# Optimization experiments

Hardware: AMD Instinct MI355X
Metric: run time of the kernel (lower is better)

Reference implementation:

```python
import jax, jax.numpy as jnp
import numpy as np

EPS = 1e-7  # K.epsilon()

def squash(s):
    # s: [B, J, D]
    sq_norm = jnp.sum(jnp.square(s), axis=-1, keepdims=True)
    scale = sq_norm / (1.0 + sq_norm) / jnp.sqrt(sq_norm + EPS)
    return scale * s

def setup_inputs() -> dict:
    key = jax.random.key(0)
    k1, k2 = jax.random.split(key)
    B, I, Din = 128, 2048, 8
    J, D = 16, 16
    inputs = jax.random.normal(k1, (B, I, Din), dtype=jnp.float32)
    # glorot-uniform-ish scale for W
    limit = np.sqrt(6.0 / (Din + D)).astype(np.float32)
    W = jax.random.uniform(k2, (J, I, D, Din), dtype=jnp.float32, minval=-limit, maxval=limit)
    return {"inputs": inputs, "W": W}

def reference(inputs, W):
    # inputs: [B, I, Din]; W: [J, I, D, Din]
    num_routings = 3
    # inputs_hat[b,j,i,d] = sum_f W[j,i,d,f] * inputs[b,i,f]
    u_hat = jnp.einsum('bif,jidf->bjid', inputs, W)  # [B, J, I, D]
    B, J, I, D = u_hat.shape
    b = jnp.zeros((B, J, I), dtype=u_hat.dtype)
    v = None
    for r in range(num_routings):
        c = jax.nn.softmax(b, axis=1)                 # softmax over output capsules (dim=1)
        s = jnp.einsum('bji,bjid->bjd', c, u_hat)     # weighted sum over input capsules
        v = squash(s)                                 # [B, J, D]
        if r < num_routings - 1:
            b = b + jnp.einsum('bjd,bjid->bji', v, u_hat)  # agreement update
    return v
```

## Files before the change

### kernel.cpp

```cpp
#include <hip/hip_runtime.h>
#include <math.h>

#define B_   128
#define I_   2048
#define F_   8
#define J_   16
#define D_   16
#define JD   256
#define IT   16
#define NIT  (I_/IT)
#define BT   16
#define NBG  (B_/BT)
#define SROW 257

typedef _Float16 f16;
typedef _Float16 f16x8 __attribute__((ext_vector_type(8)));
typedef float    f32x4 __attribute__((ext_vector_type(4)));

#if defined(__has_builtin)
#  if __has_builtin(__builtin_amdgcn_permlane32_swap)
#    define HAVE_PLS32 1
#  endif
#endif

template <int CTRL>
__device__ __forceinline__ float dpp_add(float v) {
    int t = __builtin_amdgcn_update_dpp(0, __float_as_int(v), CTRL, 0xF, 0xF, true);
    return v + __int_as_float(t);
}
__device__ __forceinline__ float row_sum16(float v) {
    v = dpp_add<0x128>(v);
    v = dpp_add<0x124>(v);
    v = dpp_add<0x122>(v);
    v = dpp_add<0x121>(v);
    return v;
}

__device__ __forceinline__ float fold16(float p) {
    return p + __int_as_float(__builtin_amdgcn_ds_swizzle(__float_as_int(p), 0x401F));
}
__device__ __forceinline__ float fold32(float p) {
#ifdef HAVE_PLS32
    auto r = __builtin_amdgcn_permlane32_swap(__float_as_int(p), __float_as_int(p),
                                              false, false);
    return __int_as_float(r[0]) + __int_as_float(r[1]);
#else
    return p + __shfl_xor(p, 32);
#endif
}

__device__ __forceinline__ f16x8 cvt8(float4 a0, float4 a1) {
    f16x8 h = {(f16)a0.x, (f16)a0.y, (f16)a0.z, (f16)a0.w,
               (f16)a1.x, (f16)a1.y, (f16)a1.z, (f16)a1.w};
    return h;
}

__global__ __launch_bounds__(256) void caps_pass0(
    const float* __restrict__ Wf,
    const float* __restrict__ xf,
    f16* __restrict__ Wt,
    f16* __restrict__ xt,
    f16* __restrict__ sp)
{
    const int it = blockIdx.x, bg = blockIdx.y;
    const int i0 = it * IT, b0 = bg * BT;
    const int t = threadIdx.x;
    const int w = t >> 6, l = t & 63;
    const int lb = l & 15, lq = l >> 4;

    __shared__ f16   xlds[IT][BT][F_];
    __shared__ float slds[BT * SROW];

    {
        const int b = t >> 4, i = t & 15;
        const size_t off = ((size_t)(b0 + b) * I_ + i0 + i) * F_;
        const float4* src = reinterpret_cast<const float4*>(xf + off);
        f16x8 h = cvt8(src[0], src[1]);
        *reinterpret_cast<f16x8*>(xt + off) = h;
        *reinterpret_cast<f16x8*>(&xlds[i][b][0]) = h;
    }
    __syncthreads();

    const f32x4 zero = {0.f, 0.f, 0.f, 0.f};
    f32x4 sacc[4] = {zero, zero, zero, zero};

    #pragma unroll
    for (int m = 0; m < 4; ++m) {
        const int i = m * 4 + lq;
        f16x8 xv = *reinterpret_cast<const f16x8*>(&xlds[i][lb][0]);
        #pragma unroll
        for (int jj = 0; jj < 4; ++jj) {
            const size_t off =
                (((size_t)(w * 4 + jj) * I_ + i0 + i) * D_ + lb) * F_;
            const float4* sw = reinterpret_cast<const float4*>(Wf + off);
            f16x8 af = cvt8(sw[0], sw[1]);
            if (bg == 0) *reinterpret_cast<f16x8*>(Wt + off) = af;
            sacc[jj] = __builtin_amdgcn_mfma_f32_16x16x32_f16(
                af, xv, sacc[jj], 0, 0, 0);
        }
    }

    #pragma unroll
    for (int jj = 0; jj < 4; ++jj) {
        f32x4 sv = sacc[jj] * 0.0625f;
        const int j = w * 4 + jj;
        #pragma unroll
        for (int r = 0; r < 4; ++r)
            slds[lb * SROW + j * D_ + lq * 4 + r] = sv[r];
    }
    __syncthreads();
    {
        const int b = t >> 4, seg = t & 15;
        float o[16];
        #pragma unroll
        for (int k = 0; k < 16; ++k)
            o[k] = slds[b * SROW + seg * 16 + k];
        f16x8 o0 = {(f16)o[0], (f16)o[1], (f16)o[2],  (f16)o[3],
                    (f16)o[4], (f16)o[5], (f16)o[6],  (f16)o[7]};
        f16x8 o1 = {(f16)o[8], (f16)o[9], (f16)o[10], (f16)o[11],
                    (f16)o[12], (f16)o[13], (f16)o[14], (f16)o[15]};
        f16* dst = sp + ((size_t)it * B_ + b0 + b) * JD + seg * 16;
        *reinterpret_cast<f16x8*>(dst) = o0;
        *reinterpret_cast<f16x8*>(dst + 8) = o1;
    }
}

__global__ __launch_bounds__(256) void caps_pass1(
    const f16* __restrict__ Wt,
    const f16* __restrict__ xt,
    const float* __restrict__ vsum,
    f16* __restrict__ sp)
{
    const int it = blockIdx.x, bg = blockIdx.y;
    const int i0 = it * IT, b0 = bg * BT;
    const int t = threadIdx.x;
    const int w = t >> 6, l = t & 63;
    const int lb = l & 15, lq = l >> 4;

    __shared__ f16 xlds[IT][BT][F_];
    __shared__ union {
        float cl[J_ * IT * BT];
        float slds[BT * SROW];
    } sh;

    {
        const int b = t >> 4, i = t & 15;
        f16x8 v = *reinterpret_cast<const f16x8*>(
            xt + ((size_t)(b0 + b) * I_ + i0 + i) * F_);
        *reinterpret_cast<f16x8*>(&xlds[i][b][0]) = v;
    }

    const f16* wp[4];
    #pragma unroll
    for (int jj = 0; jj < 4; ++jj)
        wp[jj] = Wt + (((size_t)(w * 4 + jj) * I_ + i0) * D_ + lb) * F_;

    const f32x4 zero = {0.f, 0.f, 0.f, 0.f};
    f32x4 sacc[4] = {zero, zero, zero, zero};

    float4 vr[4];
    #pragma unroll
    for (int jj = 0; jj < 4; ++jj)
        vr[jj] = *reinterpret_cast<const float4*>(
            vsum + (size_t)(b0 + lb) * JD + (w * 4 + jj) * D_ + lq * 4);
    __syncthreads();

    #pragma unroll 4
    for (int il = 0; il < IT; ++il) {
        f16x8 bf = {0, 0, 0, 0, 0, 0, 0, 0};
        if (l < 16) bf = *reinterpret_cast<const f16x8*>(&xlds[il][lb][0]);
        #pragma unroll
        for (int jj = 0; jj < 4; ++jj) {
            f16x8 af = *reinterpret_cast<const f16x8*>(wp[jj] + il * (D_ * F_));
            f32x4 u = __builtin_amdgcn_mfma_f32_16x16x32_f16(af, bf, zero, 0, 0, 0);
            float p = u[0] * vr[jj].x + u[1] * vr[jj].y +
                      u[2] * vr[jj].z + u[3] * vr[jj].w;
            p = fold32(fold16(p));
            if (l < 16) sh.cl[(((w * 4 + jj) * IT) + il) * BT + lb] = p;
        }
    }
    __syncthreads();

    {
        const int i = t >> 4, b = t & 15;
        float e[J_];
        float mx = -1e30f;
        #pragma unroll
        for (int j = 0; j < J_; ++j) {
            e[j] = sh.cl[(j * IT + i) * BT + b];
            mx = fmaxf(mx, e[j]);
        }
        float ssum = 0.f;
        #pragma unroll
        for (int j = 0; j < J_; ++j) { e[j] = __expf(e[j] - mx); ssum += e[j]; }
        const float inv = 1.f / ssum;
        #pragma unroll
        for (int j = 0; j < J_; ++j) sh.cl[(j * IT + i) * BT + b] = e[j] * inv;
    }
    __syncthreads();

    #pragma unroll
    for (int m = 0; m < 4; ++m) {
        const int i = m * 4 + lq;
        f16x8 xv = *reinterpret_cast<const f16x8*>(&xlds[i][lb][0]);
        #pragma unroll
        for (int jj = 0; jj < 4; ++jj) {
            const f16 ch = (f16)sh.cl[(((w * 4 + jj) * IT) + i) * BT + lb];
            f16x8 bf = xv * ch;
            f16x8 af = *reinterpret_cast<const f16x8*>(wp[jj] + i * (D_ * F_));
            sacc[jj] = __builtin_amdgcn_mfma_f32_16x16x32_f16(
                af, bf, sacc[jj], 0, 0, 0);
        }
    }
    __syncthreads();

    #pragma unroll
    for (int jj = 0; jj < 4; ++jj) {
        const int j = w * 4 + jj;
        #pragma unroll
        for (int r = 0; r < 4; ++r)
            sh.slds[lb * SROW + j * D_ + lq * 4 + r] = sacc[jj][r];
    }
    __syncthreads();
    {
        const int b = t >> 4, seg = t & 15;
        float o[16];
        #pragma unroll
        for (int k = 0; k < 16; ++k)
            o[k] = sh.slds[b * SROW + seg * 16 + k];
        f16x8 o0 = {(f16)o[0], (f16)o[1], (f16)o[2],  (f16)o[3],
                    (f16)o[4], (f16)o[5], (f16)o[6],  (f16)o[7]};
        f16x8 o1 = {(f16)o[8], (f16)o[9], (f16)o[10], (f16)o[11],
                    (f16)o[12], (f16)o[13], (f16)o[14], (f16)o[15]};
        f16* dst = sp + ((size_t)it * B_ + b0 + b) * JD + seg * 16;
        *reinterpret_cast<f16x8*>(dst) = o0;
        *reinterpret_cast<f16x8*>(dst + 8) = o1;
    }
}

template <int MODE>
__global__ __launch_bounds__(512) void caps_reduce(
    const f16* __restrict__ sp,
    const float* __restrict__ vA,
    float* __restrict__ vout)
{
    const int b = blockIdx.x, jh = blockIdx.y;
    const int t = threadIdx.x;
    const int g = t >> 4, c8 = t & 15;
    constexpr int ITS = NIT / 32;

    float acc[8] = {0.f, 0.f, 0.f, 0.f, 0.f, 0.f, 0.f, 0.f};
    const f16* base = sp + ((size_t)(g * ITS) * B_ + b) * JD + jh * 128 + c8 * 8;
    #pragma unroll
    for (int k = 0; k < ITS; ++k) {
        f16x8 v = *reinterpret_cast<const f16x8*>(base + (size_t)k * B_ * JD);
        #pragma unroll
        for (int e = 0; e < 8; ++e) acc[e] += (float)v[e];
    }

    __shared__ float lds[32][128];
    #pragma unroll
    for (int e = 0; e < 8; ++e) lds[g][c8 * 8 + e] = acc[e];
    __syncthreads();

    if (t < 128) {
        float a = 0.f;
        #pragma unroll
        for (int gg = 0; gg < 32; ++gg) a += lds[gg][t];
        const float sq = row_sum16(a * a);
        const float scale = sq / (1.f + sq) * rsqrtf(sq + 1e-7f);
        float v = scale * a;
        const int jd = jh * 128 + t;
        if (MODE == 1) v += vA[(size_t)b * JD + jd];
        vout[(size_t)b * JD + jd] = v;
    }
}

extern "C" void kernel_launch(void* const* d_in, const int* in_sizes, int n_in,
                              void* d_out, int out_size, void* d_ws,
                              size_t ws_size, hipStream_t stream) {
    const float* x = (const float*)d_in[0];
    const float* W = (const float*)d_in[1];
    float* out = (float*)d_out;

    const size_t NW = (size_t)J_ * I_ * D_ * F_;
    const size_t NX = (size_t)B_ * I_ * F_;
    const size_t NSP = (size_t)NIT * B_ * JD;

    f16* Wt = (f16*)d_ws;
    f16* xt = Wt + NW;
    f16* sp = xt + NX;
    float* vA = (float*)(sp + NSP);
    float* vB = vA + (size_t)B_ * JD;

    dim3 grid(NIT, NBG), blk(256);
    dim3 rgrid(B_, 2), rblk(512);

    caps_pass0<<<grid, blk, 0, stream>>>(W, x, Wt, xt, sp);
    caps_reduce<0><<<rgrid, rblk, 0, stream>>>(sp, nullptr, vA);
    caps_pass1<<<grid, blk, 0, stream>>>(Wt, xt, vA, sp);
    caps_reduce<1><<<rgrid, rblk, 0, stream>>>(sp, vA, vB);
    caps_pass1<<<grid, blk, 0, stream>>>(Wt, xt, vB, sp);
    caps_reduce<2><<<rgrid, rblk, 0, stream>>>(sp, nullptr, out);
}
```

Before: 82.33 us.

## Fuse cross-block reduction into pass kernels via last-arriver atomic ticket

Drops the three separate caps_reduce launches. Each pass kernel now takes an atomic ticket at its end, and the last 64 blocks to arrive spin until all blocks finish, then perform the reduction and squash for two batch rows each. This removes launch gaps and the tail of the separate reduce kernels, at the cost of a memset launch, spin-waiting blocks, and a reduction carried out by only 64 blocks.

```diff
diff --git a/kernel.cpp b/kernel.cpp
--- a/kernel.cpp
+++ b/kernel.cpp
@@ -11,6 +11,9 @@
 #define NIT  (I_/IT)
 #define BT   16
 #define NBG  (B_/BT)
+#define GRID_TOT (NIT*NBG)
+#define NRED 64
+#define RB   2
 #define SROW 257
 
 typedef _Float16 f16;
@@ -22,19 +25,6 @@
 #    define HAVE_PLS32 1
 #  endif
 #endif
-
-template <int CTRL>
-__device__ __forceinline__ float dpp_add(float v) {
-    int t = __builtin_amdgcn_update_dpp(0, __float_as_int(v), CTRL, 0xF, 0xF, true);
-    return v + __int_as_float(t);
-}
-__device__ __forceinline__ float row_sum16(float v) {
-    v = dpp_add<0x128>(v);
-    v = dpp_add<0x124>(v);
-    v = dpp_add<0x122>(v);
-    v = dpp_add<0x121>(v);
-    return v;
-}
 
 __device__ __forceinline__ float fold16(float p) {
     return p + __int_as_float(__builtin_amdgcn_ds_swizzle(__float_as_int(p), 0x401F));
@@ -55,12 +45,82 @@
     return h;
 }
 
+template <int MODE>
+__device__ __forceinline__ void tail_reduce(
+    const f16* __restrict__ sp,
+    const float* __restrict__ vAin,
+    float* __restrict__ vout,
+    int* __restrict__ cnt,
+    float* __restrict__ scratch,
+    int* __restrict__ tick_s,
+    const int t)
+{
+    __syncthreads();
+    if (t == 0)
+        *tick_s = __hip_atomic_fetch_add(cnt, 1, __ATOMIC_ACQ_REL,
+                                         __HIP_MEMORY_SCOPE_AGENT);
+    __syncthreads();
+    const int ticket = *tick_s;
+    if (ticket < GRID_TOT - NRED) return;
+
+    if (t == 0) {
+        while (__hip_atomic_load(cnt, __ATOMIC_ACQUIRE,
+                                 __HIP_MEMORY_SCOPE_AGENT) < GRID_TOT)
+            __builtin_amdgcn_s_sleep(8);
+    }
+    __syncthreads();
+
+    const int rblk = ticket - (GRID_TOT - NRED);
+    const int q = t >> 6, c = t & 63;
+    const int bb = c >> 5, jd8 = c & 31;
+    const int b = rblk * RB + bb;
+
+    float acc[8] = {0.f, 0.f, 0.f, 0.f, 0.f, 0.f, 0.f, 0.f};
+    const f16* base = sp + ((size_t)(q * 32) * B_ + b) * JD + jd8 * 8;
+    #pragma unroll 8
+    for (int k = 0; k < 32; ++k) {
+        f16x8 v = *reinterpret_cast<const f16x8*>(base + (size_t)k * B_ * JD);
+        #pragma unroll
+        for (int e = 0; e < 8; ++e) acc[e] += (float)v[e];
+    }
+    #pragma unroll
+    for (int e = 0; e < 8; ++e) scratch[(q * 64 + c) * 9 + e] = acc[e];
+    __syncthreads();
+
+    if (q == 0) {
+        #pragma unroll
+        for (int qq = 1; qq < 4; ++qq)
+            #pragma unroll
+            for (int e = 0; e < 8; ++e)
+                acc[e] += scratch[(qq * 64 + c) * 9 + e];
+        float sq = 0.f;
+        #pragma unroll
+        for (int e = 0; e < 8; ++e) sq = fmaf(acc[e], acc[e], sq);
+        sq += __shfl_xor(sq, 1);
+        const float scale = sq / (1.f + sq) * rsqrtf(sq + 1e-7f);
+        float v[8];
+        #pragma unroll
+        for (int e = 0; e < 8; ++e) v[e] = scale * acc[e];
+        const size_t o = (size_t)b * JD + jd8 * 8;
+        if (MODE == 1) {
+            #pragma unroll
+            for (int e = 0; e < 8; ++e) v[e] += vAin[o + e];
+        }
+        float4 v0 = {v[0], v[1], v[2], v[3]};
+        float4 v1 = {v[4], v[5], v[6], v[7]};
+        *reinterpret_cast<float4*>(vout + o) = v0;
+        *reinterpret_cast<float4*>(vout + o + 4) = v1;
+    }
+}
+
 __global__ __launch_bounds__(256) void caps_pass0(
     const float* __restrict__ Wf,
     const float* __restrict__ xf,
     f16* __restrict__ Wt,
     f16* __restrict__ xt,
-    f16* __restrict__ sp)
+    f16* __restrict__ sp,
+    float* __restrict__ vA,
+    int* __restrict__ cnt)
 {
     const int it = blockIdx.x, bg = blockIdx.y;
     const int i0 = it * IT, b0 = bg * BT;
@@ -70,6 +130,7 @@
 
     __shared__ f16   xlds[IT][BT][F_];
     __shared__ float slds[BT * SROW];
+    __shared__ int   tick_s;
 
     {
         const int b = t >> 4, i = t & 15;
@@ -123,13 +184,18 @@
         *reinterpret_cast<f16x8*>(dst) = o0;
         *reinterpret_cast<f16x8*>(dst + 8) = o1;
     }
-}
-
+
+    tail_reduce<0>(sp, nullptr, vA, cnt, slds, &tick_s, t);
+}
+
+template <int MODE>
 __global__ __launch_bounds__(256) void caps_pass1(
     const f16* __restrict__ Wt,
     const f16* __restrict__ xt,
     const float* __restrict__ vsum,
-    f16* __restrict__ sp)
+    f16* __restrict__ sp,
+    float* __restrict__ vout,
+    int* __restrict__ cnt)
 {
     const int it = blockIdx.x, bg = blockIdx.y;
     const int i0 = it * IT, b0 = bg * BT;
@@ -142,6 +208,7 @@
         float cl[J_ * IT * BT];
         float slds[BT * SROW];
     } sh;
+    __shared__ int tick_s;
 
     {
         const int b = t >> 4, i = t & 15;
@@ -236,44 +303,8 @@
         *reinterpret_cast<f16x8*>(dst) = o0;
         *reinterpret_cast<f16x8*>(dst + 8) = o1;
     }
-}
-
-template <int MODE>
-__global__ __launch_bounds__(512) void caps_reduce(
-    const f16* __restrict__ sp,
-    const float* __restrict__ vA,
-    float* __restrict__ vout)
-{
-    const int b = blockIdx.x, jh = blockIdx.y;
-    const int t = threadIdx.x;
-    const int g = t >> 4, c8 = t & 15;
-    constexpr int ITS = NIT / 32;
-
-    float acc[8] = {0.f, 0.f, 0.f, 0.f, 0.f, 0.f, 0.f, 0.f};
-    const f16* base = sp + ((size_t)(g * ITS) * B_ + b) * JD + jh * 128 + c8 * 8;
-    #pragma unroll
-    for (int k = 0; k < ITS; ++k) {
-        f16x8 v = *reinterpret_cast<const f16x8*>(base + (size_t)k * B_ * JD);
-        #pragma unroll
-        for (int e = 0; e < 8; ++e) acc[e] += (float)v[e];
-    }
-
-    __shared__ float lds[32][128];
-    #pragma unroll
-    for (int e = 0; e < 8; ++e) lds[g][c8 * 8 + e] = acc[e];
-    __syncthreads();
-
-    if (t < 128) {
-        float a = 0.f;
-        #pragma unroll
-        for (int gg = 0; gg < 32; ++gg) a += lds[gg][t];
-        const float sq = row_sum16(a * a);
-        const float scale = sq / (1.f + sq) * rsqrtf(sq + 1e-7f);
-        float v = scale * a;
-        const int jd = jh * 128 + t;
-        if (MODE == 1) v += vA[(size_t)b * JD + jd];
-        vout[(size_t)b * JD + jd] = v;
-    }
+
+    tail_reduce<MODE>(sp, vsum, vout, cnt, sh.slds, &tick_s, t);
 }
 
 extern "C" void kernel_launch(void* const* d_in, const int* in_sizes, int n_in,
@@ -292,14 +323,13 @@
     f16* sp = xt + NX;
     float* vA = (float*)(sp + NSP);
     float* vB = vA + (size_t)B_ * JD;
+    int* cnt = (int*)(vB + (size_t)B_ * JD);
+
+    hipMemsetAsync(cnt, 0, 3 * sizeof(int), stream);
 
     dim3 grid(NIT, NBG), blk(256);
-    dim3 rgrid(B_, 2), rblk(512);
-
-    caps_pass0<<<grid, blk, 0, stream>>>(W, x, Wt, xt, sp);
-    caps_reduce<0><<<rgrid, rblk, 0, stream>>>(sp, nullptr, vA);
-    caps_pass1<<<grid, blk, 0, stream>>>(Wt, xt, vA, sp);
-    caps_reduce<1><<<rgrid, rblk, 0, stream>>>(sp, vA, vB);
-    caps_pass1<<<grid, blk, 0, stream>>>(Wt, xt, vB, sp);
-    caps_reduce<2><<<rgrid, rblk, 0, stream>>>(sp, nullptr, out);
-}
+
+    caps_pass0<<<grid, blk, 0, stream>>>(W, x, Wt, xt, sp, vA, cnt);
+    caps_pass1<1><<<grid, blk, 0, stream>>>(Wt, xt, vA, sp, vB, cnt + 1);
+    caps_pass1<2><<<grid, blk, 0, stream>>>(Wt, xt, vB, sp, out, cnt + 2);
+}
```

Result: slower. 241.0 us (+192.7%).

## Compute routing agreement as W^T·v then dot with x, using transposed W copy

Applied to the files above, without the earlier changes.

The agreement logits were computed by first forming u_hat = W·x per input capsule with an MFMA, then dotting with v through cross-lane folds. They are now computed by first contracting W with v via MFMA (giving a per-feature vector), then doing a scalar FMA against x held in registers. This removes the swizzle/permlane reductions and the mostly-wasted MFMAs with zero-padded operands. A new kernel writes an extra transposed fp16 copy of W every call, which adds memory traffic and a launch. The LDS arrays are padded against bank conflicts and launch bounds now request occupancy 4.

```diff
diff --git a/kernel.cpp b/kernel.cpp
--- a/kernel.cpp
+++ b/kernel.cpp
@@ -12,16 +12,12 @@
 #define BT   16
 #define NBG  (B_/BT)
 #define SROW 257
+#define CLS  17
+#define BTP  17
 
 typedef _Float16 f16;
 typedef _Float16 f16x8 __attribute__((ext_vector_type(8)));
 typedef float    f32x4 __attribute__((ext_vector_type(4)));
-
-#if defined(__has_builtin)
-#  if __has_builtin(__builtin_amdgcn_permlane32_swap)
-#    define HAVE_PLS32 1
-#  endif
-#endif
 
 template <int CTRL>
 __device__ __forceinline__ float dpp_add(float v) {
@@ -36,23 +32,38 @@
     return v;
 }
 
-__device__ __forceinline__ float fold16(float p) {
-    return p + __int_as_float(__builtin_amdgcn_ds_swizzle(__float_as_int(p), 0x401F));
-}
-__device__ __forceinline__ float fold32(float p) {
-#ifdef HAVE_PLS32
-    auto r = __builtin_amdgcn_permlane32_swap(__float_as_int(p), __float_as_int(p),
-                                              false, false);
-    return __int_as_float(r[0]) + __int_as_float(r[1]);
-#else
-    return p + __shfl_xor(p, 32);
-#endif
-}
-
 __device__ __forceinline__ f16x8 cvt8(float4 a0, float4 a1) {
     f16x8 h = {(f16)a0.x, (f16)a0.y, (f16)a0.z, (f16)a0.w,
                (f16)a1.x, (f16)a1.y, (f16)a1.z, (f16)a1.w};
     return h;
+}
+
+__global__ __launch_bounds__(256) void cvt_wp(const float* __restrict__ Wf,
+                                              f16* __restrict__ Wp) {
+    __shared__ float wlds[32 * 129];
+    const int t = threadIdx.x;
+    const size_t base = (size_t)blockIdx.x * (32 * 128);
+
+    #pragma unroll
+    for (int q = 0; q < 4; ++q) {
+        const int idx = (q * 256 + t) * 4;
+        float4 a = *reinterpret_cast<const float4*>(Wf + base + idx);
+        const int row = idx >> 7, off = idx & 127;
+        *reinterpret_cast<float4*>(&wlds[row * 129 + off]) = a;
+    }
+    __syncthreads();
+
+    const int tile = t >> 3, f = t & 7;
+    float o[16];
+    #pragma unroll
+    for (int d = 0; d < 16; ++d) o[d] = wlds[tile * 129 + d * 8 + f];
+    f16x8 h0 = {(f16)o[0], (f16)o[1], (f16)o[2],  (f16)o[3],
+                (f16)o[4], (f16)o[5], (f16)o[6],  (f16)o[7]};
+    f16x8 h1 = {(f16)o[8], (f16)o[9], (f16)o[10], (f16)o[11],
+                (f16)o[12], (f16)o[13], (f16)o[14], (f16)o[15]};
+    f16* dst = Wp + base + (size_t)tile * 128 + f * 16;
+    *reinterpret_cast<f16x8*>(dst) = h0;
+    *reinterpret_cast<f16x8*>(dst + 8) = h1;
 }
 
 __global__ __launch_bounds__(256) void caps_pass0(
@@ -125,8 +136,9 @@
     }
 }
 
-__global__ __launch_bounds__(256) void caps_pass1(
+__global__ __launch_bounds__(256, 4) void caps_pass1(
     const f16* __restrict__ Wt,
+    const f16* __restrict__ Wp,
     const f16* __restrict__ xt,
     const float* __restrict__ vsum,
     f16* __restrict__ sp)
@@ -137,9 +149,9 @@
     const int w = t >> 6, l = t & 63;
     const int lb = l & 15, lq = l >> 4;
 
-    __shared__ f16 xlds[IT][BT][F_];
+    __shared__ f16 xlds[IT][BTP][F_];
     __shared__ union {
-        float cl[J_ * IT * BT];
+        float cl[J_ * IT * CLS];
         float slds[BT * SROW];
     } sh;
 
@@ -149,35 +161,42 @@
             xt + ((size_t)(b0 + b) * I_ + i0 + i) * F_);
         *reinterpret_cast<f16x8*>(&xlds[i][b][0]) = v;
     }
-
-    const f16* wp[4];
-    #pragma unroll
-    for (int jj = 0; jj < 4; ++jj)
-        wp[jj] = Wt + (((size_t)(w * 4 + jj) * I_ + i0) * D_ + lb) * F_;
+    __syncthreads();
 
     const f32x4 zero = {0.f, 0.f, 0.f, 0.f};
-    f32x4 sacc[4] = {zero, zero, zero, zero};
-
-    float4 vr[4];
-    #pragma unroll
-    for (int jj = 0; jj < 4; ++jj)
-        vr[jj] = *reinterpret_cast<const float4*>(
-            vsum + (size_t)(b0 + lb) * JD + (w * 4 + jj) * D_ + lq * 4);
-    __syncthreads();
-
-    #pragma unroll 4
-    for (int il = 0; il < IT; ++il) {
-        f16x8 bf = {0, 0, 0, 0, 0, 0, 0, 0};
-        if (l < 16) bf = *reinterpret_cast<const f16x8*>(&xlds[il][lb][0]);
-        #pragma unroll
-        for (int jj = 0; jj < 4; ++jj) {
-            f16x8 af = *reinterpret_cast<const f16x8*>(wp[jj] + il * (D_ * F_));
-            f32x4 u = __builtin_amdgcn_mfma_f32_16x16x32_f16(af, bf, zero, 0, 0, 0);
-            float p = u[0] * vr[jj].x + u[1] * vr[jj].y +
-                      u[2] * vr[jj].z + u[3] * vr[jj].w;
-            p = fold32(fold16(p));
-            if (l < 16) sh.cl[(((w * 4 + jj) * IT) + il) * BT + lb] = p;
+
+    f16x8 xv8[4];
+    float xfv[4][8];
+    #pragma unroll
+    for (int r = 0; r < 4; ++r) {
+        xv8[r] = *reinterpret_cast<const f16x8*>(&xlds[lq * 4 + r][lb][0]);
+        #pragma unroll
+        for (int f = 0; f < 8; ++f) xfv[r][f] = (float)xv8[r][f];
+    }
+
+    #pragma unroll
+    for (int jj = 0; jj < 4; ++jj) {
+        const int j = w * 4 + jj;
+        const float* vbp = vsum + (size_t)(b0 + lb) * JD + j * D_ + (lq & 1) * 8;
+        float4 v0 = *reinterpret_cast<const float4*>(vbp);
+        float4 v1 = *reinterpret_cast<const float4*>(vbp + 4);
+        f16x8 va8 = cvt8(v0, v1);
+        if (lq >= 2) va8 = (f16x8){0, 0, 0, 0, 0, 0, 0, 0};
+
+        const f16* wpj = Wp + ((size_t)j * I_ + i0) * (D_ * F_);
+        float L4[4] = {0.f, 0.f, 0.f, 0.f};
+        #pragma unroll
+        for (int f = 0; f < 8; ++f) {
+            f16x8 af = *reinterpret_cast<const f16x8*>(
+                wpj + lb * (D_ * F_) + f * D_ + (lq & 1) * 8);
+            f32x4 T = __builtin_amdgcn_mfma_f32_16x16x32_f16(af, va8, zero, 0, 0, 0);
+            #pragma unroll
+            for (int r = 0; r < 4; ++r)
+                L4[r] = fmaf(T[r], xfv[r][f], L4[r]);
         }
+        #pragma unroll
+        for (int r = 0; r < 4; ++r)
+            sh.cl[(j * IT + lq * 4 + r) * CLS + lb] = L4[r];
     }
     __syncthreads();
 
@@ -187,7 +206,7 @@
         float mx = -1e30f;
         #pragma unroll
         for (int j = 0; j < J_; ++j) {
-            e[j] = sh.cl[(j * IT + i) * BT + b];
+            e[j] = sh.cl[(j * IT + i) * CLS + b];
             mx = fmaxf(mx, e[j]);
         }
         float ssum = 0.f;
@@ -195,19 +214,22 @@
         for (int j = 0; j < J_; ++j) { e[j] = __expf(e[j] - mx); ssum += e[j]; }
         const float inv = 1.f / ssum;
         #pragma unroll
-        for (int j = 0; j < J_; ++j) sh.cl[(j * IT + i) * BT + b] = e[j] * inv;
-    }
-    __syncthreads();
-
+        for (int j = 0; j < J_; ++j) sh.cl[(j * IT + i) * CLS + b] = e[j] * inv;
+    }
+    __syncthreads();
+
+    f32x4 sacc[4] = {zero, zero, zero, zero};
     #pragma unroll
     for (int m = 0; m < 4; ++m) {
         const int i = m * 4 + lq;
         f16x8 xv = *reinterpret_cast<const f16x8*>(&xlds[i][lb][0]);
         #pragma unroll
         for (int jj = 0; jj < 4; ++jj) {
-            const f16 ch = (f16)sh.cl[(((w * 4 + jj) * IT) + i) * BT + lb];
+            const int j = w * 4 + jj;
+            const f16 ch = (f16)sh.cl[(j * IT + i) * CLS + lb];
             f16x8 bf = xv * ch;
-            f16x8 af = *reinterpret_cast<const f16x8*>(wp[jj] + i * (D_ * F_));
+            f16x8 af = *reinterpret_cast<const f16x8*>(
+                Wt + (((size_t)j * I_ + i0 + i) * D_ + lb) * F_);
             sacc[jj] = __builtin_amdgcn_mfma_f32_16x16x32_f16(
                 af, bf, sacc[jj], 0, 0, 0);
         }
@@ -288,7 +310,8 @@
     const size_t NSP = (size_t)NIT * B_ * JD;
 
     f16* Wt = (f16*)d_ws;
-    f16* xt = Wt + NW;
+    f16* Wp = Wt + NW;
+    f16* xt = Wp + NW;
     f16* sp = xt + NX;
     float* vA = (float*)(sp + NSP);
     float* vB = vA + (size_t)B_ * JD;
@@ -296,10 +319,12 @@
     dim3 grid(NIT, NBG), blk(256);
     dim3 rgrid(B_, 2), rblk(512);
 
+    cvt_wp<<<(int)(NW / (32 * 128)), 256, 0, stream>>>(W, Wp);
+
     caps_pass0<<<grid, blk, 0, stream>>>(W, x, Wt, xt, sp);
     caps_reduce<0><<<rgrid, rblk, 0, stream>>>(sp, nullptr, vA);
-    caps_pass1<<<grid, blk, 0, stream>>>(Wt, xt, vA, sp);
+    caps_pass1<<<grid, blk, 0, stream>>>(Wt, Wp, xt, vA, sp);
     caps_reduce<1><<<rgrid, rblk, 0, stream>>>(sp, vA, vB);
-    caps_pass1<<<grid, blk, 0, stream>>>(Wt, xt, vB, sp);
+    caps_pass1<<<grid, blk, 0, stream>>>(Wt, Wp, xt, vB, sp);
     caps_reduce<2><<<rgrid, rblk, 0, stream>>>(sp, nullptr, out);
 }
```

After: 89.30 us. +8.5%, slower.

## Widen caps_pass1 batch tile to 32 and reuse W fragments across halves

Applied to the files above, without the earlier changes.

Each caps_pass1 block now covers 32 batch rows with 512 threads (8 waves × 2 output capsules) instead of 16 rows with 256 threads (4 waves × 4 capsules). Every loaded W fragment feeds two MFMAs, one per 16-row batch half, which halves W global reads per batch row in both routing passes. The logits buffer gets a padded stride of 33 to limit LDS bank conflicts for the 32-wide layout. In exchange the grid has half as many blocks and each block uses more LDS, which can lower CU occupancy and latency hiding.

```diff
diff --git a/kernel.cpp b/kernel.cpp
--- a/kernel.cpp
+++ b/kernel.cpp
@@ -11,7 +11,10 @@
 #define NIT  (I_/IT)
 #define BT   16
 #define NBG  (B_/BT)
+#define BT2  32
+#define NBG2 (B_/BT2)
 #define SROW 257
+#define CLS  33
 
 typedef _Float16 f16;
 typedef _Float16 f16x8 __attribute__((ext_vector_type(8)));
@@ -125,22 +128,22 @@
     }
 }
 
-__global__ __launch_bounds__(256) void caps_pass1(
+__global__ __launch_bounds__(512, 4) void caps_pass1(
     const f16* __restrict__ Wt,
     const f16* __restrict__ xt,
     const float* __restrict__ vsum,
     f16* __restrict__ sp)
 {
     const int it = blockIdx.x, bg = blockIdx.y;
-    const int i0 = it * IT, b0 = bg * BT;
+    const int i0 = it * IT, b0 = bg * BT2;
     const int t = threadIdx.x;
     const int w = t >> 6, l = t & 63;
     const int lb = l & 15, lq = l >> 4;
 
-    __shared__ f16 xlds[IT][BT][F_];
+    __shared__ f16 xlds[IT][BT2][F_];
     __shared__ union {
-        float cl[J_ * IT * BT];
-        float slds[BT * SROW];
+        float cl[J_ * IT * CLS];
+        float slds[BT2 * SROW];
     } sh;
 
     {
@@ -150,44 +153,58 @@
         *reinterpret_cast<f16x8*>(&xlds[i][b][0]) = v;
     }
 
-    const f16* wp[4];
-    #pragma unroll
-    for (int jj = 0; jj < 4; ++jj)
-        wp[jj] = Wt + (((size_t)(w * 4 + jj) * I_ + i0) * D_ + lb) * F_;
+    const f16* wp[2];
+    #pragma unroll
+    for (int jj = 0; jj < 2; ++jj)
+        wp[jj] = Wt + (((size_t)(w * 2 + jj) * I_ + i0) * D_ + lb) * F_;
 
     const f32x4 zero = {0.f, 0.f, 0.f, 0.f};
-    f32x4 sacc[4] = {zero, zero, zero, zero};
-
-    float4 vr[4];
-    #pragma unroll
-    for (int jj = 0; jj < 4; ++jj)
-        vr[jj] = *reinterpret_cast<const float4*>(
-            vsum + (size_t)(b0 + lb) * JD + (w * 4 + jj) * D_ + lq * 4);
+
+    float4 vr[2][2];
+    #pragma unroll
+    for (int jj = 0; jj < 2; ++jj)
+        #pragma unroll
+        for (int bh = 0; bh < 2; ++bh)
+            vr[jj][bh] = *reinterpret_cast<const float4*>(
+                vsum + (size_t)(b0 + bh * 16 + lb) * JD +
+                (w * 2 + jj) * D_ + lq * 4);
     __syncthreads();
 
     #pragma unroll 4
     for (int il = 0; il < IT; ++il) {
-        f16x8 bf = {0, 0, 0, 0, 0, 0, 0, 0};
-        if (l < 16) bf = *reinterpret_cast<const f16x8*>(&xlds[il][lb][0]);
-        #pragma unroll
-        for (int jj = 0; jj < 4; ++jj) {
+        f16x8 bf0 = {0, 0, 0, 0, 0, 0, 0, 0};
+        f16x8 bf1 = {0, 0, 0, 0, 0, 0, 0, 0};
+        if (l < 16) {
+            bf0 = *reinterpret_cast<const f16x8*>(&xlds[il][lb][0]);
+            bf1 = *reinterpret_cast<const f16x8*>(&xlds[il][16 + lb][0]);
+        }
+        #pragma unroll
+        for (int jj = 0; jj < 2; ++jj) {
             f16x8 af = *reinterpret_cast<const f16x8*>(wp[jj] + il * (D_ * F_));
-            f32x4 u = __builtin_amdgcn_mfma_f32_16x16x32_f16(af, bf, zero, 0, 0, 0);
-            float p = u[0] * vr[jj].x + u[1] * vr[jj].y +
-                      u[2] * vr[jj].z + u[3] * vr[jj].w;
-            p = fold32(fold16(p));
-            if (l < 16) sh.cl[(((w * 4 + jj) * IT) + il) * BT + lb] = p;
-        }
-    }
-    __syncthreads();
-
-    {
-        const int i = t >> 4, b = t & 15;
+            f32x4 u0 = __builtin_amdgcn_mfma_f32_16x16x32_f16(af, bf0, zero, 0, 0, 0);
+            float p0 = u0[0] * vr[jj][0].x + u0[1] * vr[jj][0].y +
+                       u0[2] * vr[jj][0].z + u0[3] * vr[jj][0].w;
+            p0 = fold32(fold16(p0));
+            f32x4 u1 = __builtin_amdgcn_mfma_f32_16x16x32_f16(af, bf1, zero, 0, 0, 0);
+            float p1 = u1[0] * vr[jj][1].x + u1[1] * vr[jj][1].y +
+                       u1[2] * vr[jj][1].z + u1[3] * vr[jj][1].w;
+            p1 = fold32(fold16(p1));
+            if (l < 16) {
+                const int j = w * 2 + jj;
+                sh.cl[(j * IT + il) * CLS + lb] = p0;
+                sh.cl[(j * IT + il) * CLS + 16 + lb] = p1;
+            }
+        }
+    }
+    __syncthreads();
+
+    {
+        const int i = t >> 5, b = t & 31;
         float e[J_];
         float mx = -1e30f;
         #pragma unroll
         for (int j = 0; j < J_; ++j) {
-            e[j] = sh.cl[(j * IT + i) * BT + b];
+            e[j] = sh.cl[(j * IT + i) * CLS + b];
             mx = fmaxf(mx, e[j]);
         }
         float ssum = 0.f;
@@ -195,31 +212,41 @@
         for (int j = 0; j < J_; ++j) { e[j] = __expf(e[j] - mx); ssum += e[j]; }
         const float inv = 1.f / ssum;
         #pragma unroll
-        for (int j = 0; j < J_; ++j) sh.cl[(j * IT + i) * BT + b] = e[j] * inv;
-    }
-    __syncthreads();
-
+        for (int j = 0; j < J_; ++j) sh.cl[(j * IT + i) * CLS + b] = e[j] * inv;
+    }
+    __syncthreads();
+
+    f32x4 sacc[2][2] = {{zero, zero}, {zero, zero}};
     #pragma unroll
     for (int m = 0; m < 4; ++m) {
         const int i = m * 4 + lq;
-        f16x8 xv = *reinterpret_cast<const f16x8*>(&xlds[i][lb][0]);
-        #pragma unroll
-        for (int jj = 0; jj < 4; ++jj) {
-            const f16 ch = (f16)sh.cl[(((w * 4 + jj) * IT) + i) * BT + lb];
-            f16x8 bf = xv * ch;
+        f16x8 xv0 = *reinterpret_cast<const f16x8*>(&xlds[i][lb][0]);
+        f16x8 xv1 = *reinterpret_cast<const f16x8*>(&xlds[i][16 + lb][0]);
+        #pragma unroll
+        for (int jj = 0; jj < 2; ++jj) {
+            const int j = w * 2 + jj;
             f16x8 af = *reinterpret_cast<const f16x8*>(wp[jj] + i * (D_ * F_));
-            sacc[jj] = __builtin_amdgcn_mfma_f32_16x16x32_f16(
-                af, bf, sacc[jj], 0, 0, 0);
-        }
-    }
-    __syncthreads();
-
-    #pragma unroll
-    for (int jj = 0; jj < 4; ++jj) {
-        const int j = w * 4 + jj;
-        #pragma unroll
-        for (int r = 0; r < 4; ++r)
-            sh.slds[lb * SROW + j * D_ + lq * 4 + r] = sacc[jj][r];
+            const f16 c0 = (f16)sh.cl[(j * IT + i) * CLS + lb];
+            const f16 c1 = (f16)sh.cl[(j * IT + i) * CLS + 16 + lb];
+            f16x8 bf0 = xv0 * c0;
+            f16x8 bf1 = xv1 * c1;
+            sacc[jj][0] = __builtin_amdgcn_mfma_f32_16x16x32_f16(
+                af, bf0, sacc[jj][0], 0, 0, 0);
+            sacc[jj][1] = __builtin_amdgcn_mfma_f32_16x16x32_f16(
+                af, bf1, sacc[jj][1], 0, 0, 0);
+        }
+    }
+    __syncthreads();
+
+    #pragma unroll
+    for (int jj = 0; jj < 2; ++jj) {
+        const int j = w * 2 + jj;
+        #pragma unroll
+        for (int bh = 0; bh < 2; ++bh)
+            #pragma unroll
+            for (int r = 0; r < 4; ++r)
+                sh.slds[(bh * 16 + lb) * SROW + j * D_ + lq * 4 + r] =
+                    sacc[jj][bh][r];
     }
     __syncthreads();
     {
@@ -293,13 +320,14 @@
     float* vA = (float*)(sp + NSP);
     float* vB = vA + (size_t)B_ * JD;
 
-    dim3 grid(NIT, NBG), blk(256);
+    dim3 grid0(NIT, NBG), blk0(256);
+    dim3 grid1(NIT, NBG2), blk1(512);
     dim3 rgrid(B_, 2), rblk(512);
 
-    caps_pass0<<<grid, blk, 0, stream>>>(W, x, Wt, xt, sp);
+    caps_pass0<<<grid0, blk0, 0, stream>>>(W, x, Wt, xt, sp);
     caps_reduce<0><<<rgrid, rblk, 0, stream>>>(sp, nullptr, vA);
-    caps_pass1<<<grid, blk, 0, stream>>>(Wt, xt, vA, sp);
+    caps_pass1<<<grid1, blk1, 0, stream>>>(Wt, xt, vA, sp);
     caps_reduce<1><<<rgrid, rblk, 0, stream>>>(sp, vA, vB);
-    caps_pass1<<<grid, blk, 0, stream>>>(Wt, xt, vB, sp);
+    caps_pass1<<<grid1, blk1, 0, stream>>>(Wt, xt, vB, sp);
     caps_reduce<2><<<rgrid, rblk, 0, stream>>>(sp, nullptr, out);
 }
```

After: 70.41 us. 14.5% less time.
